# Optimization experiments

Hardware: AMD Instinct MI355X
Metric: run time of the kernel (lower is better)

The kernel has to match this reference:

```python
import jax, jax.numpy as jnp
import numpy as np

ORDER = 2        # order_in1 = order_in2 = order_out = 2
N = 60000        # number of atom pairs (edges)
F = 128          # num_features
B = 32           # num_basis_functions
TRIPLES = [(l1, l2, L) for l1 in range(ORDER + 1) for l2 in range(ORDER + 1)
           for L in range(abs(l1 - l2), min(l1 + l2, ORDER) + 1)]


def setup_inputs():
    key = jax.random.key(0)
    ks = iter(jax.random.split(key, 64))
    inp = {}
    for l in range(ORDER + 1):
        inp[f"x1_{l}"] = jax.random.normal(next(ks), (N, 2 * l + 1, F), jnp.float32)
    for l in range(ORDER + 1):
        inp[f"x2_{l}"] = jax.random.normal(next(ks), (N, 2 * l + 1, F), jnp.float32)
    inp["rbf"] = jax.random.uniform(next(ks), (N, B), jnp.float32)
    for (l1, l2, L) in TRIPLES:
        # fixed Clebsch-Gordan-like constant tensors; real CG tensors are sparse,
        cg = jax.random.normal(next(ks), (2 * l1 + 1, 2 * l2 + 1, 2 * L + 1), jnp.float32)
        mask = jax.random.uniform(next(ks), cg.shape) < 0.3
        inp[f"cg_{l1}_{l2}_{L}"] = jnp.where(mask, cg, 0.0)
        # nn.Linear(B, F, bias=False) weight has shape [F, B]
        inp[f"W_{l1}_{l2}_{L}"] = jax.random.normal(next(ks), (F, B), jnp.float32) / np.sqrt(B)
    return inp


def _pair_mixing(xs1, xs2, rbf, cgs, Ws):
    n = rbf.shape[0]
    f = xs1[0].shape[-1]
    ys = [jnp.zeros((n, 2 * L + 1, f), rbf.dtype) for L in range(ORDER + 1)]
    for i, (l1, l2, L) in enumerate(TRIPLES):
        coeff = rbf @ Ws[i].T                                           # [N, F]
        # fused CG tensor product: sum_{i,j} cg[i,j,k] * x1[n,i,f] * x2[n,j,f]
        tp = jnp.einsum('nif,njf,ijk->nkf', xs1[l1], xs2[l2], cgs[i])   # [N, 2L+1, F]
        ys[L] = ys[L] + coeff[:, None, :] * tp
    return tuple(ys)


def reference(x1_0, x1_1, x1_2, x2_0, x2_1, x2_2, rbf,
              cg_0_0_0, cg_0_1_1, cg_0_2_2, cg_1_0_1, cg_1_1_0, cg_1_1_1, cg_1_1_2,
              cg_1_2_1, cg_1_2_2, cg_2_0_2, cg_2_1_1, cg_2_1_2, cg_2_2_0, cg_2_2_1, cg_2_2_2,
              W_0_0_0, W_0_1_1, W_0_2_2, W_1_0_1, W_1_1_0, W_1_1_1, W_1_1_2,
              W_1_2_1, W_1_2_2, W_2_0_2, W_2_1_1, W_2_1_2, W_2_2_0, W_2_2_1, W_2_2_2):
    loc = locals()
    cgs = [loc[f"cg_{a}_{b}_{c}"] for (a, b, c) in TRIPLES]
    Ws = [loc[f"W_{a}_{b}_{c}"] for (a, b, c) in TRIPLES]
    return _pair_mixing([x1_0, x1_1, x1_2], [x2_0, x2_1, x2_2], rbf, cgs, Ws)
```

## Files before the change

kernel.cpp:

```cpp
#include <hip/hip_runtime.h>


#define NPAIR 60000
#define NB    8
#define Y1OFF (NPAIR * 128)
#define Y2OFF (NPAIR * 128 * 4)

template<int D1, int D2, int DK>
__device__ __forceinline__ void triple_acc(
    const float* __restrict__ cg,
    const float (&a)[D1][2], const float (&b)[D2][2],
    float cf0, float cf1, float (&y)[DK][2])
{
    float tp[DK][2];
#pragma unroll
    for (int k = 0; k < DK; ++k) { tp[k][0] = 0.f; tp[k][1] = 0.f; }
#pragma unroll
    for (int i = 0; i < D1; ++i) {
#pragma unroll
        for (int j = 0; j < D2; ++j) {
#pragma unroll
            for (int nn = 0; nn < 2; ++nn) {
                const float prod = a[i][nn] * b[j][nn];
#pragma unroll
                for (int k = 0; k < DK; ++k) {
                    tp[k][nn] = fmaf(cg[(i * D2 + j) * DK + k], prod, tp[k][nn]);
                }
            }
        }
    }
#pragma unroll
    for (int k = 0; k < DK; ++k) {
        y[k][0] = fmaf(cf0, tp[k][0], y[k][0]);
        y[k][1] = fmaf(cf1, tp[k][1], y[k][1]);
    }
}

__device__ __forceinline__ void coeff_t(
    const float* __restrict__ Wt, const float* __restrict__ rbfp,
    int f, float (&cfo)[4])
{
    const float4* wp = (const float4*)(Wt + ((size_t)f << 5));
    float wv[32];
#pragma unroll
    for (int q = 0; q < 8; ++q) {
        const float4 v = wp[q];
        wv[4 * q + 0] = v.x; wv[4 * q + 1] = v.y;
        wv[4 * q + 2] = v.z; wv[4 * q + 3] = v.w;
    }
#pragma unroll
    for (int nn = 0; nn < 4; ++nn) {
        float acc = 0.f;
#pragma unroll
        for (int b = 0; b < 32; ++b)
            acc = fmaf(rbfp[nn * 32 + b], wv[b], acc);
        cfo[nn] = acc;
    }
}

__global__ __launch_bounds__(256, 3) void pair_mixing_kernel(
    const float* __restrict__ x1_0, const float* __restrict__ x1_1, const float* __restrict__ x1_2,
    const float* __restrict__ x2_0, const float* __restrict__ x2_1, const float* __restrict__ x2_2,
    const float* __restrict__ rbf,
    const float* __restrict__ cg0,  const float* __restrict__ cg1,  const float* __restrict__ cg2,
    const float* __restrict__ cg3,  const float* __restrict__ cg4,  const float* __restrict__ cg5,
    const float* __restrict__ cg6,  const float* __restrict__ cg7,  const float* __restrict__ cg8,
    const float* __restrict__ cg9,  const float* __restrict__ cg10, const float* __restrict__ cg11,
    const float* __restrict__ cg12, const float* __restrict__ cg13, const float* __restrict__ cg14,
    const float* __restrict__ W0,  const float* __restrict__ W1,  const float* __restrict__ W2,
    const float* __restrict__ W3,  const float* __restrict__ W4,  const float* __restrict__ W5,
    const float* __restrict__ W6,  const float* __restrict__ W7,  const float* __restrict__ W8,
    const float* __restrict__ W9,  const float* __restrict__ W10, const float* __restrict__ W11,
    const float* __restrict__ W12, const float* __restrict__ W13, const float* __restrict__ W14,
    float* __restrict__ out)
{
    const int tid = threadIdx.x;
    const int f   = tid & 127;
    const int sub = tid >> 7;
    const int nbt = blockIdx.x * NB + sub * 4;
    const int nbu = __builtin_amdgcn_readfirstlane(nbt);
    const float* rbfp = rbf + ((size_t)nbu << 5);

    float cf[15][4];
    coeff_t(W0,  rbfp, f, cf[0]);
    coeff_t(W1,  rbfp, f, cf[1]);
    coeff_t(W2,  rbfp, f, cf[2]);
    coeff_t(W3,  rbfp, f, cf[3]);
    coeff_t(W4,  rbfp, f, cf[4]);
    coeff_t(W5,  rbfp, f, cf[5]);
    coeff_t(W6,  rbfp, f, cf[6]);
    coeff_t(W7,  rbfp, f, cf[7]);
    coeff_t(W8,  rbfp, f, cf[8]);
    coeff_t(W9,  rbfp, f, cf[9]);
    coeff_t(W10, rbfp, f, cf[10]);
    coeff_t(W11, rbfp, f, cf[11]);
    coeff_t(W12, rbfp, f, cf[12]);
    coeff_t(W13, rbfp, f, cf[13]);
    coeff_t(W14, rbfp, f, cf[14]);

#pragma unroll
    for (int pass = 0; pass < 2; ++pass) {
        const int nb = nbt + pass * 2;

        float a0[1][2], a1[3][2], a2[5][2];
        float c0[1][2], c1[3][2], c2[5][2];
#pragma unroll
        for (int nn = 0; nn < 2; ++nn) {
            const int n = nb + nn;
            a0[0][nn] = x1_0[n * 128 + f];
#pragma unroll
            for (int i = 0; i < 3; ++i) a1[i][nn] = x1_1[(n * 3 + i) * 128 + f];
#pragma unroll
            for (int i = 0; i < 5; ++i) a2[i][nn] = x1_2[(n * 5 + i) * 128 + f];
            c0[0][nn] = x2_0[n * 128 + f];
#pragma unroll
            for (int j = 0; j < 3; ++j) c1[j][nn] = x2_1[(n * 3 + j) * 128 + f];
#pragma unroll
            for (int j = 0; j < 5; ++j) c2[j][nn] = x2_2[(n * 5 + j) * 128 + f];
        }

        float y0v[1][2], y1v[3][2], y2v[5][2];
#pragma unroll
        for (int k = 0; k < 1; ++k) { y0v[k][0] = 0.f; y0v[k][1] = 0.f; }
#pragma unroll
        for (int k = 0; k < 3; ++k) { y1v[k][0] = 0.f; y1v[k][1] = 0.f; }
#pragma unroll
        for (int k = 0; k < 5; ++k) { y2v[k][0] = 0.f; y2v[k][1] = 0.f; }

        const int p0 = 2 * pass, p1 = 2 * pass + 1;
        triple_acc<1,1,1>(cg0,  a0, c0, cf[0][p0],  cf[0][p1],  y0v);
        triple_acc<1,3,3>(cg1,  a0, c1, cf[1][p0],  cf[1][p1],  y1v);
        triple_acc<1,5,5>(cg2,  a0, c2, cf[2][p0],  cf[2][p1],  y2v);
        triple_acc<3,1,3>(cg3,  a1, c0, cf[3][p0],  cf[3][p1],  y1v);
        triple_acc<3,3,1>(cg4,  a1, c1, cf[4][p0],  cf[4][p1],  y0v);
        triple_acc<3,3,3>(cg5,  a1, c1, cf[5][p0],  cf[5][p1],  y1v);
        triple_acc<3,3,5>(cg6,  a1, c1, cf[6][p0],  cf[6][p1],  y2v);
        triple_acc<3,5,3>(cg7,  a1, c2, cf[7][p0],  cf[7][p1],  y1v);
        triple_acc<3,5,5>(cg8,  a1, c2, cf[8][p0],  cf[8][p1],  y2v);
        triple_acc<5,1,5>(cg9,  a2, c0, cf[9][p0],  cf[9][p1],  y2v);
        triple_acc<5,3,3>(cg10, a2, c1, cf[10][p0], cf[10][p1], y1v);
        triple_acc<5,3,5>(cg11, a2, c1, cf[11][p0], cf[11][p1], y2v);
        triple_acc<5,5,1>(cg12, a2, c2, cf[12][p0], cf[12][p1], y0v);
        triple_acc<5,5,3>(cg13, a2, c2, cf[13][p0], cf[13][p1], y1v);
        triple_acc<5,5,5>(cg14, a2, c2, cf[14][p0], cf[14][p1], y2v);

#pragma unroll
        for (int nn = 0; nn < 2; ++nn) {
            const int n = nb + nn;
            out[n * 128 + f] = y0v[0][nn];
#pragma unroll
            for (int k = 0; k < 3; ++k)
                out[Y1OFF + (n * 3 + k) * 128 + f] = y1v[k][nn];
#pragma unroll
            for (int k = 0; k < 5; ++k)
                out[Y2OFF + (n * 5 + k) * 128 + f] = y2v[k][nn];
        }
    }
}

extern "C" void kernel_launch(void* const* d_in, const int* in_sizes, int n_in,
                              void* d_out, int out_size, void* d_ws, size_t ws_size,
                              hipStream_t stream) {
    const float* x1_0 = (const float*)d_in[0];
    const float* x1_1 = (const float*)d_in[1];
    const float* x1_2 = (const float*)d_in[2];
    const float* x2_0 = (const float*)d_in[3];
    const float* x2_1 = (const float*)d_in[4];
    const float* x2_2 = (const float*)d_in[5];
    const float* rbf  = (const float*)d_in[6];
    const float* cg[15];
    const float* W[15];
    for (int t = 0; t < 15; ++t) {
        cg[t] = (const float*)d_in[7 + 2 * t];
        W[t]  = (const float*)d_in[8 + 2 * t];
    }
    float* out = (float*)d_out;

    dim3 grid(NPAIR / NB);
    dim3 block(256);
    pair_mixing_kernel<<<grid, block, 0, stream>>>(
        x1_0, x1_1, x1_2, x2_0, x2_1, x2_2, rbf,
        cg[0], cg[1], cg[2], cg[3], cg[4], cg[5], cg[6], cg[7],
        cg[8], cg[9], cg[10], cg[11], cg[12], cg[13], cg[14],
        W[0], W[1], W[2], W[3], W[4], W[5], W[6], W[7],
        W[8], W[9], W[10], W[11], W[12], W[13], W[14],
        out);
}
```

Measured before the change: 1.118 ms.

## Halve pairs per thread, chunk coefficient GEMV, and load inputs early

Each thread now processes two pairs instead of four, and the block covers four pairs. The rbf·W coefficient computation is split into chunks of eight basis functions, interleaved across all 15 weights. The x1/x2 loads are issued before the coefficient compute so their latency can overlap. This cuts register pressure and raises the occupancy target, but W weights are now reused over fewer pairs, doubling weight load traffic per pair.

```diff
diff --git a/kernel.cpp b/kernel.cpp
--- a/kernel.cpp
+++ b/kernel.cpp
@@ -2,7 +2,7 @@
 
 
 #define NPAIR 60000
-#define NB    8
+#define NB    4
 #define Y1OFF (NPAIR * 128)
 #define Y2OFF (NPAIR * 128 * 4)
 
@@ -36,29 +36,7 @@
     }
 }
 
-__device__ __forceinline__ void coeff_t(
-    const float* __restrict__ Wt, const float* __restrict__ rbfp,
-    int f, float (&cfo)[4])
-{
-    const float4* wp = (const float4*)(Wt + ((size_t)f << 5));
-    float wv[32];
-#pragma unroll
-    for (int q = 0; q < 8; ++q) {
-        const float4 v = wp[q];
-        wv[4 * q + 0] = v.x; wv[4 * q + 1] = v.y;
-        wv[4 * q + 2] = v.z; wv[4 * q + 3] = v.w;
-    }
-#pragma unroll
-    for (int nn = 0; nn < 4; ++nn) {
-        float acc = 0.f;
-#pragma unroll
-        for (int b = 0; b < 32; ++b)
-            acc = fmaf(rbfp[nn * 32 + b], wv[b], acc);
-        cfo[nn] = acc;
-    }
-}
-
-__global__ __launch_bounds__(256, 3) void pair_mixing_kernel(
+__global__ __launch_bounds__(256, 4) void pair_mixing_kernel(
     const float* __restrict__ x1_0, const float* __restrict__ x1_1, const float* __restrict__ x1_2,
     const float* __restrict__ x2_0, const float* __restrict__ x2_1, const float* __restrict__ x2_2,
     const float* __restrict__ rbf,
@@ -77,84 +55,89 @@
     const int tid = threadIdx.x;
     const int f   = tid & 127;
     const int sub = tid >> 7;
-    const int nbt = blockIdx.x * NB + sub * 4;
-    const int nbu = __builtin_amdgcn_readfirstlane(nbt);
+    const int nb  = blockIdx.x * NB + sub * 2;
+    const int nbu = __builtin_amdgcn_readfirstlane(nb);
     const float* rbfp = rbf + ((size_t)nbu << 5);
 
-    float cf[15][4];
-    coeff_t(W0,  rbfp, f, cf[0]);
-    coeff_t(W1,  rbfp, f, cf[1]);
-    coeff_t(W2,  rbfp, f, cf[2]);
-    coeff_t(W3,  rbfp, f, cf[3]);
-    coeff_t(W4,  rbfp, f, cf[4]);
-    coeff_t(W5,  rbfp, f, cf[5]);
-    coeff_t(W6,  rbfp, f, cf[6]);
-    coeff_t(W7,  rbfp, f, cf[7]);
-    coeff_t(W8,  rbfp, f, cf[8]);
-    coeff_t(W9,  rbfp, f, cf[9]);
-    coeff_t(W10, rbfp, f, cf[10]);
-    coeff_t(W11, rbfp, f, cf[11]);
-    coeff_t(W12, rbfp, f, cf[12]);
-    coeff_t(W13, rbfp, f, cf[13]);
-    coeff_t(W14, rbfp, f, cf[14]);
+    float a0[1][2], a1[3][2], a2[5][2];
+    float c0[1][2], c1[3][2], c2[5][2];
+#pragma unroll
+    for (int nn = 0; nn < 2; ++nn) {
+        const int n = nb + nn;
+        a0[0][nn] = x1_0[n * 128 + f];
+#pragma unroll
+        for (int i = 0; i < 3; ++i) a1[i][nn] = x1_1[(n * 3 + i) * 128 + f];
+#pragma unroll
+        for (int i = 0; i < 5; ++i) a2[i][nn] = x1_2[(n * 5 + i) * 128 + f];
+        c0[0][nn] = x2_0[n * 128 + f];
+#pragma unroll
+        for (int j = 0; j < 3; ++j) c1[j][nn] = x2_1[(n * 3 + j) * 128 + f];
+#pragma unroll
+        for (int j = 0; j < 5; ++j) c2[j][nn] = x2_2[(n * 5 + j) * 128 + f];
+    }
+
+    const float* Wt[15] = {W0, W1, W2, W3, W4, W5, W6, W7,
+                           W8, W9, W10, W11, W12, W13, W14};
+    float cf[15][2];
+#pragma unroll
+    for (int t = 0; t < 15; ++t) { cf[t][0] = 0.f; cf[t][1] = 0.f; }
 
 #pragma unroll
-    for (int pass = 0; pass < 2; ++pass) {
-        const int nb = nbt + pass * 2;
+    for (int ch = 0; ch < 4; ++ch) {
+        float rb0[8], rb1[8];
+#pragma unroll
+        for (int b = 0; b < 8; ++b) {
+            rb0[b] = rbfp[ch * 8 + b];
+            rb1[b] = rbfp[32 + ch * 8 + b];
+        }
+#pragma unroll
+        for (int t = 0; t < 15; ++t) {
+            const float4* wp = (const float4*)(Wt[t] + ((size_t)f << 5) + ch * 8);
+            const float4 w0 = wp[0];
+            const float4 w1 = wp[1];
+            const float wv[8] = {w0.x, w0.y, w0.z, w0.w, w1.x, w1.y, w1.z, w1.w};
+#pragma unroll
+            for (int b = 0; b < 8; ++b) {
+                cf[t][0] = fmaf(rb0[b], wv[b], cf[t][0]);
+                cf[t][1] = fmaf(rb1[b], wv[b], cf[t][1]);
+            }
+        }
+    }
 
-        float a0[1][2], a1[3][2], a2[5][2];
-        float c0[1][2], c1[3][2], c2[5][2];
+    float y0v[1][2], y1v[3][2], y2v[5][2];
 #pragma unroll
-        for (int nn = 0; nn < 2; ++nn) {
-            const int n = nb + nn;
-            a0[0][nn] = x1_0[n * 128 + f];
+    for (int k = 0; k < 1; ++k) { y0v[k][0] = 0.f; y0v[k][1] = 0.f; }
 #pragma unroll
-            for (int i = 0; i < 3; ++i) a1[i][nn] = x1_1[(n * 3 + i) * 128 + f];
+    for (int k = 0; k < 3; ++k) { y1v[k][0] = 0.f; y1v[k][1] = 0.f; }
 #pragma unroll
-            for (int i = 0; i < 5; ++i) a2[i][nn] = x1_2[(n * 5 + i) * 128 + f];
-            c0[0][nn] = x2_0[n * 128 + f];
-#pragma unroll
-            for (int j = 0; j < 3; ++j) c1[j][nn] = x2_1[(n * 3 + j) * 128 + f];
-#pragma unroll
-            for (int j = 0; j < 5; ++j) c2[j][nn] = x2_2[(n * 5 + j) * 128 + f];
-        }
+    for (int k = 0; k < 5; ++k) { y2v[k][0] = 0.f; y2v[k][1] = 0.f; }
 
-        float y0v[1][2], y1v[3][2], y2v[5][2];
-#pragma unroll
-        for (int k = 0; k < 1; ++k) { y0v[k][0] = 0.f; y0v[k][1] = 0.f; }
-#pragma unroll
-        for (int k = 0; k < 3; ++k) { y1v[k][0] = 0.f; y1v[k][1] = 0.f; }
-#pragma unroll
-        for (int k = 0; k < 5; ++k) { y2v[k][0] = 0.f; y2v[k][1] = 0.f; }
-
-        const int p0 = 2 * pass, p1 = 2 * pass + 1;
-        triple_acc<1,1,1>(cg0,  a0, c0, cf[0][p0],  cf[0][p1],  y0v);
-        triple_acc<1,3,3>(cg1,  a0, c1, cf[1][p0],  cf[1][p1],  y1v);
-        triple_acc<1,5,5>(cg2,  a0, c2, cf[2][p0],  cf[2][p1],  y2v);
-        triple_acc<3,1,3>(cg3,  a1, c0, cf[3][p0],  cf[3][p1],  y1v);
-        triple_acc<3,3,1>(cg4,  a1, c1, cf[4][p0],  cf[4][p1],  y0v);
-        triple_acc<3,3,3>(cg5,  a1, c1, cf[5][p0],  cf[5][p1],  y1v);
-        triple_acc<3,3,5>(cg6,  a1, c1, cf[6][p0],  cf[6][p1],  y2v);
-        triple_acc<3,5,3>(cg7,  a1, c2, cf[7][p0],  cf[7][p1],  y1v);
-        triple_acc<3,5,5>(cg8,  a1, c2, cf[8][p0],  cf[8][p1],  y2v);
-        triple_acc<5,1,5>(cg9,  a2, c0, cf[9][p0],  cf[9][p1],  y2v);
-        triple_acc<5,3,3>(cg10, a2, c1, cf[10][p0], cf[10][p1], y1v);
-        triple_acc<5,3,5>(cg11, a2, c1, cf[11][p0], cf[11][p1], y2v);
-        triple_acc<5,5,1>(cg12, a2, c2, cf[12][p0], cf[12][p1], y0v);
-        triple_acc<5,5,3>(cg13, a2, c2, cf[13][p0], cf[13][p1], y1v);
-        triple_acc<5,5,5>(cg14, a2, c2, cf[14][p0], cf[14][p1], y2v);
+    triple_acc<1,1,1>(cg0,  a0, c0, cf[0][0],  cf[0][1],  y0v);
+    triple_acc<1,3,3>(cg1,  a0, c1, cf[1][0],  cf[1][1],  y1v);
+    triple_acc<1,5,5>(cg2,  a0, c2, cf[2][0],  cf[2][1],  y2v);
+    triple_acc<3,1,3>(cg3,  a1, c0, cf[3][0],  cf[3][1],  y1v);
+    triple_acc<3,3,1>(cg4,  a1, c1, cf[4][0],  cf[4][1],  y0v);
+    triple_acc<3,3,3>(cg5,  a1, c1, cf[5][0],  cf[5][1],  y1v);
+    triple_acc<3,3,5>(cg6,  a1, c1, cf[6][0],  cf[6][1],  y2v);
+    triple_acc<3,5,3>(cg7,  a1, c2, cf[7][0],  cf[7][1],  y1v);
+    triple_acc<3,5,5>(cg8,  a1, c2, cf[8][0],  cf[8][1],  y2v);
+    triple_acc<5,1,5>(cg9,  a2, c0, cf[9][0],  cf[9][1],  y2v);
+    triple_acc<5,3,3>(cg10, a2, c1, cf[10][0], cf[10][1], y1v);
+    triple_acc<5,3,5>(cg11, a2, c1, cf[11][0], cf[11][1], y2v);
+    triple_acc<5,5,1>(cg12, a2, c2, cf[12][0], cf[12][1], y0v);
+    triple_acc<5,5,3>(cg13, a2, c2, cf[13][0], cf[13][1], y1v);
+    triple_acc<5,5,5>(cg14, a2, c2, cf[14][0], cf[14][1], y2v);
 
 #pragma unroll
-        for (int nn = 0; nn < 2; ++nn) {
-            const int n = nb + nn;
-            out[n * 128 + f] = y0v[0][nn];
+    for (int nn = 0; nn < 2; ++nn) {
+        const int n = nb + nn;
+        out[n * 128 + f] = y0v[0][nn];
 #pragma unroll
-            for (int k = 0; k < 3; ++k)
-                out[Y1OFF + (n * 3 + k) * 128 + f] = y1v[k][nn];
+        for (int k = 0; k < 3; ++k)
+            out[Y1OFF + (n * 3 + k) * 128 + f] = y1v[k][nn];
 #pragma unroll
-            for (int k = 0; k < 5; ++k)
-                out[Y2OFF + (n * 5 + k) * 128 + f] = y2v[k][nn];
-        }
+        for (int k = 0; k < 5; ++k)
+            out[Y2OFF + (n * 5 + k) * 128 + f] = y2v[k][nn];
     }
 }
 
```

Measured after the change: 2.158 ms. 1.93x slower.

## Transpose W into coalesced workspace layout and restructure coefficient loop for occupancy

Applied to the files above, without the earlier changes.

Adds a small pre-kernel that transposes all fifteen W matrices into a workspace laid out so that adjacent threads (features) read adjacent float4s, making the weight loads coalesced. The coefficient computation is reordered to loop over basis chunks outermost, loading only four W values at a time instead of a 32-float register array per triple. This cuts register pressure, and the launch bound is raised from 3 to 4 waves per SIMD. The cost is an extra kernel launch and a workspace dependency, with a fallback path that uses the original layout when no workspace is available.

```diff
diff --git a/kernel.cpp b/kernel.cpp
--- a/kernel.cpp
+++ b/kernel.cpp
@@ -5,6 +5,18 @@
 #define NB    8
 #define Y1OFF (NPAIR * 128)
 #define Y2OFF (NPAIR * 128 * 4)
+#define WT_BYTES (15 * 128 * 32 * 4)
+
+struct WPtrs { const float* w[15]; };
+
+__global__ void transpose_W_kernel(WPtrs P, float* __restrict__ WT) {
+    const int t  = blockIdx.y;
+    const int id = blockIdx.x * 256 + threadIdx.x;
+    const int f  = id >> 3;
+    const int q  = id & 7;
+    const float4 v = ((const float4*)(P.w[t] + f * 32))[q];
+    ((float4*)WT)[(t * 8 + q) * 128 + f] = v;
+}
 
 template<int D1, int D2, int DK>
 __device__ __forceinline__ void triple_acc(
@@ -36,29 +48,8 @@
     }
 }
 
-__device__ __forceinline__ void coeff_t(
-    const float* __restrict__ Wt, const float* __restrict__ rbfp,
-    int f, float (&cfo)[4])
-{
-    const float4* wp = (const float4*)(Wt + ((size_t)f << 5));
-    float wv[32];
-#pragma unroll
-    for (int q = 0; q < 8; ++q) {
-        const float4 v = wp[q];
-        wv[4 * q + 0] = v.x; wv[4 * q + 1] = v.y;
-        wv[4 * q + 2] = v.z; wv[4 * q + 3] = v.w;
-    }
-#pragma unroll
-    for (int nn = 0; nn < 4; ++nn) {
-        float acc = 0.f;
-#pragma unroll
-        for (int b = 0; b < 32; ++b)
-            acc = fmaf(rbfp[nn * 32 + b], wv[b], acc);
-        cfo[nn] = acc;
-    }
-}
-
-__global__ __launch_bounds__(256, 3) void pair_mixing_kernel(
+template<bool USE_WT>
+__global__ __launch_bounds__(256, 4) void pair_mixing_kernel(
     const float* __restrict__ x1_0, const float* __restrict__ x1_1, const float* __restrict__ x1_2,
     const float* __restrict__ x2_0, const float* __restrict__ x2_1, const float* __restrict__ x2_2,
     const float* __restrict__ rbf,
@@ -72,6 +63,7 @@
     const float* __restrict__ W6,  const float* __restrict__ W7,  const float* __restrict__ W8,
     const float* __restrict__ W9,  const float* __restrict__ W10, const float* __restrict__ W11,
     const float* __restrict__ W12, const float* __restrict__ W13, const float* __restrict__ W14,
+    const float* __restrict__ WT,
     float* __restrict__ out)
 {
     const int tid = threadIdx.x;
@@ -81,22 +73,38 @@
     const int nbu = __builtin_amdgcn_readfirstlane(nbt);
     const float* rbfp = rbf + ((size_t)nbu << 5);
 
+    const float* Wt[15] = {W0, W1, W2, W3, W4, W5, W6, W7,
+                           W8, W9, W10, W11, W12, W13, W14};
     float cf[15][4];
-    coeff_t(W0,  rbfp, f, cf[0]);
-    coeff_t(W1,  rbfp, f, cf[1]);
-    coeff_t(W2,  rbfp, f, cf[2]);
-    coeff_t(W3,  rbfp, f, cf[3]);
-    coeff_t(W4,  rbfp, f, cf[4]);
-    coeff_t(W5,  rbfp, f, cf[5]);
-    coeff_t(W6,  rbfp, f, cf[6]);
-    coeff_t(W7,  rbfp, f, cf[7]);
-    coeff_t(W8,  rbfp, f, cf[8]);
-    coeff_t(W9,  rbfp, f, cf[9]);
-    coeff_t(W10, rbfp, f, cf[10]);
-    coeff_t(W11, rbfp, f, cf[11]);
-    coeff_t(W12, rbfp, f, cf[12]);
-    coeff_t(W13, rbfp, f, cf[13]);
-    coeff_t(W14, rbfp, f, cf[14]);
+#pragma unroll
+    for (int t = 0; t < 15; ++t)
+#pragma unroll
+        for (int nn = 0; nn < 4; ++nn) cf[t][nn] = 0.f;
+
+#pragma unroll
+    for (int q = 0; q < 8; ++q) {
+        float rb[4][4];
+#pragma unroll
+        for (int nn = 0; nn < 4; ++nn)
+#pragma unroll
+            for (int r = 0; r < 4; ++r)
+                rb[nn][r] = rbfp[nn * 32 + q * 4 + r];
+#pragma unroll
+        for (int t = 0; t < 15; ++t) {
+            float4 w;
+            if (USE_WT) {
+                w = ((const float4*)WT)[(t * 8 + q) * 128 + f];
+            } else {
+                w = ((const float4*)(Wt[t] + ((size_t)f << 5)))[q];
+            }
+            const float wv[4] = {w.x, w.y, w.z, w.w};
+#pragma unroll
+            for (int r = 0; r < 4; ++r)
+#pragma unroll
+                for (int nn = 0; nn < 4; ++nn)
+                    cf[t][nn] = fmaf(rb[nn][r], wv[r], cf[t][nn]);
+        }
+    }
 
 #pragma unroll
     for (int pass = 0; pass < 2; ++pass) {
@@ -176,13 +184,29 @@
     }
     float* out = (float*)d_out;
 
+    const bool use_wt = (d_ws != nullptr) && (ws_size >= (size_t)WT_BYTES);
+
     dim3 grid(NPAIR / NB);
     dim3 block(256);
-    pair_mixing_kernel<<<grid, block, 0, stream>>>(
-        x1_0, x1_1, x1_2, x2_0, x2_1, x2_2, rbf,
-        cg[0], cg[1], cg[2], cg[3], cg[4], cg[5], cg[6], cg[7],
-        cg[8], cg[9], cg[10], cg[11], cg[12], cg[13], cg[14],
-        W[0], W[1], W[2], W[3], W[4], W[5], W[6], W[7],
-        W[8], W[9], W[10], W[11], W[12], W[13], W[14],
-        out);
-}
+
+    if (use_wt) {
+        WPtrs P;
+        for (int t = 0; t < 15; ++t) P.w[t] = W[t];
+        transpose_W_kernel<<<dim3(4, 15), dim3(256), 0, stream>>>(P, (float*)d_ws);
+        pair_mixing_kernel<true><<<grid, block, 0, stream>>>(
+            x1_0, x1_1, x1_2, x2_0, x2_1, x2_2, rbf,
+            cg[0], cg[1], cg[2], cg[3], cg[4], cg[5], cg[6], cg[7],
+            cg[8], cg[9], cg[10], cg[11], cg[12], cg[13], cg[14],
+            W[0], W[1], W[2], W[3], W[4], W[5], W[6], W[7],
+            W[8], W[9], W[10], W[11], W[12], W[13], W[14],
+            (const float*)d_ws, out);
+    } else {
+        pair_mixing_kernel<false><<<grid, block, 0, stream>>>(
+            x1_0, x1_1, x1_2, x2_0, x2_1, x2_2, rbf,
+            cg[0], cg[1], cg[2], cg[3], cg[4], cg[5], cg[6], cg[7],
+            cg[8], cg[9], cg[10], cg[11], cg[12], cg[13], cg[14],
+            W[0], W[1], W[2], W[3], W[4], W[5], W[6], W[7],
+            W[8], W[9], W[10], W[11], W[12], W[13], W[14],
+            nullptr, out);
+    }
+}
```

After: 1.124 ms. Within noise of the previous version (+0.5%).
